# Kernel tuning notes

Measured on AMD Instinct MI355X. Metric: run time of the kernel, lower is better.

Reference implementation:

```python
import jax, jax.numpy as jnp
import numpy as np

B, D, K = 32768, 256, 8192
COMMITMENT_COST = 0.25
DECAY = 0.99
EPS = 1e-05


def setup_inputs() -> dict:
    key = jax.random.key(0)
    k1, k2, k3, k4 = jax.random.split(key, 4)
    z = jax.random.normal(k1, (B, D), dtype=jnp.float32)
    embedding = jax.random.normal(k2, (K, D), dtype=jnp.float32)
    ema_cluster_size = jnp.ones((K,), dtype=jnp.float32)
    ema_embedding_sum = embedding.copy()
    # pre-sampled randomness for dead-code reinitialization (one slot per code)
    reinit_noise = jax.random.normal(k3, (K, D), dtype=jnp.float32) * 0.1
    reinit_idx = jax.random.randint(k4, (K,), 0, B)
    return {
        "z": z,
        "embedding": embedding,
        "ema_cluster_size": ema_cluster_size,
        "ema_embedding_sum": ema_embedding_sum,
        "reinit_noise": reinit_noise,
        "reinit_idx": reinit_idx,
    }


def reference(z, embedding, ema_cluster_size, ema_embedding_sum, reinit_noise, reinit_idx):
    # squared L2 distances: [B, K]
    distances = (
        jnp.sum(z * z, axis=1, keepdims=True)
        + jnp.sum(embedding * embedding, axis=1)
        - 2.0 * jnp.matmul(z, embedding.T)
    )
    indices = jnp.argmin(distances, axis=1)  # [B]
    z_q = embedding[indices]                  # [B, D]

    # EMA codebook update (training-mode math), one-hot scatter via segment_sum
    ones = jnp.ones((z.shape[0],), dtype=z.dtype)
    cluster_size = jax.ops.segment_sum(ones, indices, num_segments=K)       # [K]
    embedding_sum = jax.ops.segment_sum(z, indices, num_segments=K)          # [K, D]
    new_ema_cs = DECAY * ema_cluster_size + (1.0 - DECAY) * cluster_size
    new_ema_es = DECAY * ema_embedding_sum + (1.0 - DECAY) * embedding_sum
    n = jnp.sum(new_ema_cs)
    cs_smoothed = (new_ema_cs + EPS) / (n + K * EPS) * n
    new_embedding = new_ema_es / cs_smoothed[:, None]

    # dead-code reinitialization (masked, fixed-shape)
    usage = new_ema_cs / n
    dead = usage < (1.0 / K / 10.0)           # [K] bool
    reinit = z[reinit_idx] + reinit_noise     # [K, D]
    new_embedding = jnp.where(dead[:, None], reinit, new_embedding)
    new_ema_cs = jnp.where(dead, 1.0, new_ema_cs)
    new_ema_es = jnp.where(dead[:, None], reinit, new_ema_es)

    # losses / metrics
    commitment_loss = COMMITMENT_COST * jnp.mean((jax.lax.stop_gradient(z_q) - z) ** 2)
    z_q_st = z + jax.lax.stop_gradient(z_q - z)  # straight-through
    avg_probs = cluster_size / z.shape[0]
    perplexity = jnp.exp(-jnp.sum(avg_probs * jnp.log(avg_probs + 1e-10)))

    return (z_q_st, commitment_loss, indices, perplexity, new_embedding, new_ema_cs, new_ema_es)
```

## Files before the change

kernel.cpp:

```cpp
#include <hip/hip_runtime.h>
#include <math.h>

#define BN 32768
#define DN 256
#define KN 8192
#define CCAP 20

#define O_LOSS 8388608
#define O_IDX  8388609
#define O_PERP 8421377
#define O_EMB  8421378
#define O_CS   10518530
#define O_ES   10526722

typedef _Float16 half_t;
typedef __attribute__((ext_vector_type(4))) _Float16 half4v;
typedef __attribute__((ext_vector_type(8))) _Float16 half8;
typedef __attribute__((ext_vector_type(16))) float float16v;
typedef unsigned long long u64;
typedef unsigned int u32;

__device__ __forceinline__ float wave_reduce_add(float v) {
#pragma unroll
  for (int off = 32; off > 0; off >>= 1) v += __shfl_down(v, off);
  return v;
}

__device__ __forceinline__ u32 enc_f(float d) {
  u32 fb = __float_as_uint(d);
  return fb ^ ((fb >> 31) ? 0xFFFFFFFFu : 0x80000000u);
}

__global__ __launch_bounds__(256) void k_prep_z(const float* __restrict__ z,
                                                half_t* __restrict__ zh,
                                                float* __restrict__ znh,
                                                float* __restrict__ znl) {
  const int wid = threadIdx.x >> 6, lane = threadIdx.x & 63;
  const int row = blockIdx.x * 4 + wid;
  float4 v = *(const float4*)(z + (size_t)row * DN + lane * 4);
  float xs[4] = {v.x, v.y, v.z, v.w};
  half4v hv;
  float h2 = 0.f, l2 = 0.f;
#pragma unroll
  for (int j = 0; j < 4; ++j) {
    half_t hh = (half_t)xs[j];
    float lf = xs[j] - (float)hh;
    hv[j] = hh;
    h2 += (float)hh * (float)hh;
    l2 += lf * lf;
  }
  const int tile = row >> 7, r = row & 127, kg = lane >> 1, off = (lane & 1) * 4;
  *(half4v*)(zh + (size_t)tile * 32768 + kg * 1024 + r * 8 + off) = hv;
#pragma unroll
  for (int o = 32; o > 0; o >>= 1) {
    h2 += __shfl_down(h2, o);
    l2 += __shfl_down(l2, o);
  }
  if (lane == 0) {
    znh[row] = sqrtf(h2);
    znl[row] = sqrtf(l2);
  }
}

__global__ __launch_bounds__(256) void k_prep_e(const float* __restrict__ e,
                                                half_t* __restrict__ eh,
                                                float* __restrict__ enorm,
                                                float* __restrict__ emaxp) {
  __shared__ float mh[4], ml[4];
  const int wid = threadIdx.x >> 6, lane = threadIdx.x & 63;
  const int row = blockIdx.x * 4 + wid;
  float4 v = *(const float4*)(e + (size_t)row * DN + lane * 4);
  float xs[4] = {v.x, v.y, v.z, v.w};
  half4v hv;
  float h2 = 0.f, l2 = 0.f, x2 = 0.f;
#pragma unroll
  for (int j = 0; j < 4; ++j) {
    half_t hh = (half_t)xs[j];
    float lf = xs[j] - (float)hh;
    hv[j] = hh;
    h2 += (float)hh * (float)hh;
    l2 += lf * lf;
    x2 += xs[j] * xs[j];
  }
  const int tile = row >> 6, r = row & 63, kg = lane >> 1, off = (lane & 1) * 4;
  *(half4v*)(eh + (size_t)tile * 16384 + kg * 512 + r * 8 + off) = hv;
#pragma unroll
  for (int o = 32; o > 0; o >>= 1) {
    h2 += __shfl_down(h2, o);
    l2 += __shfl_down(l2, o);
    x2 += __shfl_down(x2, o);
  }
  if (lane == 0) {
    enorm[row] = x2;
    mh[wid] = sqrtf(h2);
    ml[wid] = sqrtf(l2);
  }
  __syncthreads();
  if (threadIdx.x == 0) {
    emaxp[blockIdx.x * 2] = fmaxf(fmaxf(mh[0], mh[1]), fmaxf(mh[2], mh[3]));
    emaxp[blockIdx.x * 2 + 1] = fmaxf(fmaxf(ml[0], ml[1]), fmaxf(ml[2], ml[3]));
  }
}

__global__ __launch_bounds__(256) void k_norm(const float* __restrict__ emaxp,
                                              float* __restrict__ Wf) {
  __shared__ float sh[256], sl[256];
  const int t = threadIdx.x;
  float vh = 0.f, vl = 0.f;
  for (int i = t; i < 2048; i += 256) {
    vh = fmaxf(vh, emaxp[i * 2]);
    vl = fmaxf(vl, emaxp[i * 2 + 1]);
  }
  sh[t] = vh;
  sl[t] = vl;
  __syncthreads();
  for (int st = 128; st > 0; st >>= 1) {
    if (t < st) {
      sh[t] = fmaxf(sh[t], sh[t + st]);
      sl[t] = fmaxf(sl[t], sl[t + st]);
    }
    __syncthreads();
  }
  if (t == 0) {
    Wf[4] = sh[0];
    Wf[5] = sl[0];
  }
}

__global__ __launch_bounds__(256, 2) void k_pass1(
    const half_t* __restrict__ eh, const half_t* __restrict__ zh,
    const float* __restrict__ z, const float* __restrict__ emb,
    const float* __restrict__ enorm, const float* __restrict__ znh,
    const float* __restrict__ znl, const float* __restrict__ Wf,
    u64* __restrict__ best, u32* __restrict__ oflow) {
  __shared__ __align__(16) half_t EB[2][8192];
  __shared__ float En_s[2048];
  __shared__ u64 clist[128 * CCAP];
  __shared__ u32 pcnt[128];
  __shared__ float rowbest[128];

  const int tid = threadIdx.x;
  const int wid = tid >> 6, lane = tid & 63;
  const int l31 = lane & 31, h = lane >> 5;
  const int zt = blockIdx.x;
  const int sp = blockIdx.y;
  const int lrow = wid * 32 + l31;
  const int grow = zt * 128 + lrow;

  for (int i = tid; i < 2048; i += 256) En_s[i] = enorm[sp * 2048 + i];
  if (tid < 128) pcnt[tid] = 0;

  half8 zr[16];
  {
    const half_t* zb = zh + (size_t)zt * 32768 + (size_t)lrow * 8;
#pragma unroll
    for (int ks = 0; ks < 16; ++ks)
      zr[ks] = *(const half8*)(zb + (size_t)(ks * 2 + h) * 1024);
  }
  const float thr2 =
      4.0f * (znh[grow] * Wf[5] + znl[grow] * (Wf[4] + Wf[5])) + 0.06f;

  const half_t* ebase = eh + ((size_t)sp << 19);
  float bestd = 3.4e38f;

#define STG(s, b)                                                              \
  {                                                                            \
    const half_t* g_ = ebase + (size_t)(s) * 8192 + wid * 2048 + lane * 8;     \
    half_t* d_ = &EB[b][wid * 2048 + lane * 8];                                \
    _Pragma("unroll") for (int i_ = 0; i_ < 4; ++i_)                           \
        __builtin_amdgcn_global_load_lds(                                      \
            (const __attribute__((address_space(1))) void*)(g_ + i_ * 512),    \
            (__attribute__((address_space(3))) void*)(d_ + i_ * 512), 16, 0,   \
            0);                                                                \
  }

  STG(0, 0)
  for (int t = 0; t < 32; ++t) {
    float16v acc0 = {}, acc1 = {};
#pragma unroll
    for (int kh = 0; kh < 2; ++kh) {
      const int s = t * 2 + kh;
      __syncthreads();
      if (s < 63) STG(s + 1, (s + 1) & 1)
      const half_t* B = EB[s & 1];
#pragma unroll
      for (int ks = 0; ks < 8; ++ks) {
        const int ko = (ks * 2 + h) * 512;
        half8 a0 = *(const half8*)(B + ko + l31 * 8);
        half8 a1 = *(const half8*)(B + ko + (32 + l31) * 8);
        acc0 = __builtin_amdgcn_mfma_f32_32x32x16_f16(a0, zr[kh * 8 + ks],
                                                      acc0, 0, 0, 0);
        acc1 = __builtin_amdgcn_mfma_f32_32x32x16_f16(a1, zr[kh * 8 + ks],
                                                      acc1, 0, 0, 0);
      }
    }
    float ds[32];
    float tmin = 3.4e38f;
#pragma unroll
    for (int mi = 0; mi < 2; ++mi) {
      const float16v a = mi ? acc1 : acc0;
#pragma unroll
      for (int r = 0; r < 16; ++r) {
        const int cl = t * 64 + mi * 32 + (r & 3) + 8 * (r >> 2) + 4 * h;
        const float d = En_s[cl] - 2.0f * a[r];
        ds[mi * 16 + r] = d;
        tmin = d < tmin ? d : tmin;
      }
    }
    {
      float o = __shfl_xor(tmin, 32);
      tmin = o < tmin ? o : tmin;
      bestd = tmin < bestd ? tmin : bestd;
    }
    const float lim = bestd + thr2;
#pragma unroll
    for (int mi = 0; mi < 2; ++mi)
#pragma unroll
      for (int r = 0; r < 16; ++r) {
        const float d = ds[mi * 16 + r];
        if (d <= lim) {
          const int cl = t * 64 + mi * 32 + (r & 3) + 8 * (r >> 2) + 4 * h;
          const u32 slot = atomicAdd(&pcnt[lrow], 1u);
          if (slot < CCAP)
            clist[lrow * CCAP + slot] =
                ((u64)enc_f(d) << 32) | (u32)(sp * 2048 + cl);
        }
      }
  }
#undef STG

  if (h == 0) rowbest[lrow] = bestd;
  __syncthreads();

  for (int lr = wid; lr < 128; lr += 4) {
    const int gr = zt * 128 + lr;
    const u32 n = pcnt[lr];
    if (n > CCAP) {
      if (lane == 0) oflow[gr] = 1u;
      continue;
    }
    const float t2 =
        4.0f * (znh[gr] * Wf[5] + znl[gr] * (Wf[4] + Wf[5])) + 0.06f;
    const u32 lim = enc_f(rowbest[lr] + t2);
    u64 bk = ~0ull;
    const float4 zv = *(const float4*)(z + (size_t)gr * DN + lane * 4);
    for (u32 j = 0; j < n; ++j) {
      const u64 e = clist[lr * CCAP + j];
      if ((u32)(e >> 32) > lim) continue;
      const int c = (int)(e & 0x1FFFu);
      float4 ev = *(const float4*)(emb + (size_t)c * DN + lane * 4);
      float dot = wave_reduce_add(zv.x * ev.x + zv.y * ev.y + zv.z * ev.z +
                                  zv.w * ev.w);
      if (lane == 0) {
        const float d = enorm[c] - 2.0f * dot;
        const u64 kk = ((u64)enc_f(d) << 32) | (u32)c;
        bk = kk < bk ? kk : bk;
      }
    }
    if (lane == 0) atomicMin(best + gr, bk);
  }
}

__global__ __launch_bounds__(256) void k_out(const float* __restrict__ z,
                                             const float* __restrict__ emb,
                                             const float* __restrict__ enorm,
                                             const u64* __restrict__ best,
                                             const u32* __restrict__ oflow,
                                             float* __restrict__ out,
                                             float* __restrict__ losspart,
                                             float* __restrict__ cluster,
                                             int* __restrict__ idxp) {
  __shared__ float lp[4];
  int wid = threadIdx.x >> 6, lane = threadIdx.x & 63;
  int row = blockIdx.x * 4 + wid;
  int d = lane << 2;
  float4 zv = *(const float4*)(z + (size_t)row * DN + d);
  int k;
  if (oflow[row] != 0u) {
    u64 bk = ~0ull;
    for (int c = 0; c < KN; ++c) {
      float4 ev = *(const float4*)(emb + (size_t)c * DN + d);
      float dot = wave_reduce_add(zv.x * ev.x + zv.y * ev.y + zv.z * ev.z +
                                  zv.w * ev.w);
      if (lane == 0) {
        const float dd = enorm[c] - 2.0f * dot;
        const u64 kk = ((u64)enc_f(dd) << 32) | (u32)c;
        bk = kk < bk ? kk : bk;
      }
    }
    int k0 = (int)((u32)bk & 0x1FFFu);
    k = __shfl(k0, 0);
  } else {
    k = (int)((u32)best[row] & 0x1FFFu);
  }
  float4 ev = *(const float4*)(emb + (size_t)k * DN + d);
  float4 df = make_float4(ev.x - zv.x, ev.y - zv.y, ev.z - zv.z, ev.w - zv.w);
  float4 st = make_float4(zv.x + df.x, zv.y + df.y, zv.z + df.z, zv.w + df.w);
  *(float4*)(out + (size_t)row * DN + d) = st;
  float sq = df.x * df.x + df.y * df.y + df.z * df.z + df.w * df.w;
  sq = wave_reduce_add(sq);
  if (lane == 0) {
    lp[wid] = sq;
    unsafeAtomicAdd(&cluster[k], 1.0f);
    out[O_IDX + row] = (float)k;
    idxp[row] = k;
  }
  __syncthreads();
  if (threadIdx.x == 0)
    losspart[blockIdx.x] = lp[0] + lp[1] + lp[2] + lp[3];
}

__global__ __launch_bounds__(256) void k_scan(const float* __restrict__ ema_cs,
                                              const float* __restrict__ cluster,
                                              const float* __restrict__ losspart,
                                              float* __restrict__ newcs,
                                              int* __restrict__ rowstart,
                                              int* __restrict__ cursor,
                                              float* __restrict__ Wf) {
  __shared__ int ssum[256];
  __shared__ float sn[256], sp[256], sl[256];
  const int t = threadIdx.x;
  const int base = t * 32;
  int s = 0;
  float nsum = 0.f, plsum = 0.f, lsum = 0.f;
  for (int j = 0; j < 32; ++j) {
    float cs = cluster[base + j];
    s += (int)cs;
    float nc = 0.99f * ema_cs[base + j] + 0.01f * cs;
    newcs[base + j] = nc;
    nsum += nc;
    float p = cs * (1.0f / 32768.0f);
    plsum += p * logf(p + 1e-10f);
    lsum += losspart[base + j];
  }
  ssum[t] = s;
  sn[t] = nsum;
  sp[t] = plsum;
  sl[t] = lsum;
  __syncthreads();
  for (int st = 1; st < 256; st <<= 1) {
    int v = (t >= st) ? ssum[t - st] : 0;
    __syncthreads();
    ssum[t] += v;
    __syncthreads();
  }
  int off = ssum[t] - s;
  for (int j = 0; j < 32; ++j) {
    rowstart[base + j] = off;
    cursor[base + j] = off;
    off += (int)cluster[base + j];
  }
  for (int st = 128; st > 0; st >>= 1) {
    if (t < st) {
      sn[t] += sn[t + st];
      sp[t] += sp[t + st];
      sl[t] += sl[t + st];
    }
    __syncthreads();
  }
  if (t == 0) {
    Wf[0] = sl[0];
    Wf[1] = sn[0];
    Wf[2] = sp[0];
  }
}

__global__ __launch_bounds__(256) void k_scatter(const int* __restrict__ idxp,
                                                 int* __restrict__ cursor,
                                                 int* __restrict__ rowlist) {
  const int row = blockIdx.x * 256 + threadIdx.x;
  const int pos = atomicAdd(cursor + idxp[row], 1);
  rowlist[pos] = row;
}

__global__ __launch_bounds__(256) void k_accum(const float* __restrict__ z,
                                               const float* __restrict__ cluster,
                                               const int* __restrict__ rowstart,
                                               const int* __restrict__ rowlist,
                                               float* __restrict__ embsum) {
  const int wid = threadIdx.x >> 6, lane = threadIdx.x & 63;
  const int code = blockIdx.x * 4 + wid;
  const int cnt = (int)cluster[code];
  const int st = rowstart[code];
  float4 a = make_float4(0.f, 0.f, 0.f, 0.f);
  for (int j = 0; j < cnt; ++j) {
    const int row = rowlist[st + j];
    float4 v = *(const float4*)(z + (size_t)row * DN + lane * 4);
    a.x += v.x;
    a.y += v.y;
    a.z += v.z;
    a.w += v.w;
  }
  *(float4*)(embsum + (size_t)code * DN + lane * 4) = a;
}

__global__ __launch_bounds__(256) void k_final(const float* __restrict__ z,
                                               const float* __restrict__ ema_es,
                                               const float* __restrict__ noise,
                                               const int* __restrict__ ridx,
                                               const float* __restrict__ embsum,
                                               const float* __restrict__ newcs,
                                               const float* __restrict__ W,
                                               float* __restrict__ out) {
  int gid = blockIdx.x * 256 + threadIdx.x;
  int k = gid >> 6;
  int d = (gid & 63) << 2;
  float n = W[1];
  float nc = newcs[k];
  float cs_sm = (nc + 1e-5f) / (n + (float)KN * 1e-5f) * n;
  bool dead = (nc / n) < (1.0f / (KN * 10.0f));
  size_t o = (size_t)k * DN + d;
  float4 es = *(const float4*)(ema_es + o);
  float4 s = *(const float4*)(embsum + o);
  float4 nes = make_float4(0.99f * es.x + 0.01f * s.x, 0.99f * es.y + 0.01f * s.y,
                           0.99f * es.z + 0.01f * s.z, 0.99f * es.w + 0.01f * s.w);
  float4 ne = make_float4(nes.x / cs_sm, nes.y / cs_sm, nes.z / cs_sm,
                          nes.w / cs_sm);
  if (dead) {
    int r = ridx[k];
    float4 rz = *(const float4*)(z + (size_t)r * DN + d);
    float4 rn = *(const float4*)(noise + o);
    nes = make_float4(rz.x + rn.x, rz.y + rn.y, rz.z + rn.z, rz.w + rn.w);
    ne = nes;
  }
  float* oe = out + O_EMB + o;
  *(float2*)(oe) = make_float2(ne.x, ne.y);
  *(float2*)(oe + 2) = make_float2(ne.z, ne.w);
  float* os = out + O_ES + o;
  *(float2*)(os) = make_float2(nes.x, nes.y);
  *(float2*)(os + 2) = make_float2(nes.z, nes.w);
  if ((gid & 63) == 0) out[O_CS + k] = dead ? 1.0f : nc;
  if (gid == 0) {
    out[O_LOSS] = 0.25f * W[0] * (1.0f / 8388608.0f);
    out[O_PERP] = expf(-W[2]);
  }
}

extern "C" void kernel_launch(void* const* d_in, const int* in_sizes, int n_in,
                              void* d_out, int out_size, void* d_ws,
                              size_t ws_size, hipStream_t stream) {
  const float* z = (const float*)d_in[0];
  const float* emb = (const float*)d_in[1];
  const float* ema_cs = (const float*)d_in[2];
  const float* ema_es = (const float*)d_in[3];
  const float* noise = (const float*)d_in[4];
  const int* ridx = (const int*)d_in[5];
  float* out = (float*)d_out;

  float* Wf = (float*)d_ws;
  float* cluster = Wf + 16;
  u32* oflow = (u32*)(cluster + KN);
  float* newcs = (float*)(oflow + BN);
  float* enorm = newcs + KN;
  float* znh = enorm + KN;
  float* znl = znh + BN;
  int* rowstart = (int*)(znl + BN);
  int* cursor = rowstart + KN;
  int* rowlist = cursor + KN;
  int* idxp = rowlist + BN;
  float* losspart = (float*)(idxp + BN);
  float* emaxp = losspart + KN;
  u64* best = (u64*)(emaxp + 4096);
  float* embsum = (float*)(best + BN);

  half_t* zh = (half_t*)out;
  half_t* eh = (half_t*)(out + (size_t)BN * DN / 2);

  hipMemsetAsync(Wf, 0, (size_t)(16 + KN + BN) * sizeof(float), stream);
  hipMemsetAsync(best, 0xFF, (size_t)BN * sizeof(u64), stream);

  k_prep_z<<<BN / 4, 256, 0, stream>>>(z, zh, znh, znl);
  k_prep_e<<<KN / 4, 256, 0, stream>>>(emb, eh, enorm, emaxp);
  k_norm<<<1, 256, 0, stream>>>(emaxp, Wf);
  k_pass1<<<dim3(BN / 128, 4), 256, 0, stream>>>(eh, zh, z, emb, enorm, znh,
                                                 znl, Wf, best, oflow);
  k_out<<<BN / 4, 256, 0, stream>>>(z, emb, enorm, best, oflow, out, losspart,
                                    cluster, idxp);
  k_scan<<<1, 256, 0, stream>>>(ema_cs, cluster, losspart, newcs, rowstart,
                                cursor, Wf);
  k_scatter<<<BN / 256, 256, 0, stream>>>(idxp, cursor, rowlist);
  k_accum<<<KN / 4, 256, 0, stream>>>(z, cluster, rowstart, rowlist, embsum);
  k_final<<<(KN * 64) / 256, 256, 0, stream>>>(z, ema_es, noise, ridx, embsum,
                                               newcs, Wf, out);
}
```

Baseline: 637.1 us.

## Restructure distance GEMM to register-resident z tiles with per-wave codebook slices

The pass-1 distance kernel now processes 64 z rows per block, with two 32-row z fragments held in registers. Each wave streams its own 512-code slice of the half-precision codebook straight from global memory instead of sharing double-buffered LDS stages behind block-wide barriers. Per-row best distances are shared across waves through LDS atomicMin so candidate pruning stays tight, and the candidate cap is raised. The z and codebook prep kernels are merged into one launch using a shared 64-row tile layout. This removes LDS staging and barriers, but each block now rereads the codebook from global memory or L2 with no LDS reuse, and there are more blocks.

```diff
diff --git a/kernel.cpp b/kernel.cpp
--- a/kernel.cpp
+++ b/kernel.cpp
@@ -4,7 +4,7 @@
 #define BN 32768
 #define DN 256
 #define KN 8192
-#define CCAP 20
+#define CCAP 24
 
 #define O_LOSS 8388608
 #define O_IDX  8388609
@@ -30,46 +30,24 @@
   u32 fb = __float_as_uint(d);
   return fb ^ ((fb >> 31) ? 0xFFFFFFFFu : 0x80000000u);
 }
-
-__global__ __launch_bounds__(256) void k_prep_z(const float* __restrict__ z,
-                                                half_t* __restrict__ zh,
-                                                float* __restrict__ znh,
-                                                float* __restrict__ znl) {
-  const int wid = threadIdx.x >> 6, lane = threadIdx.x & 63;
-  const int row = blockIdx.x * 4 + wid;
-  float4 v = *(const float4*)(z + (size_t)row * DN + lane * 4);
-  float xs[4] = {v.x, v.y, v.z, v.w};
-  half4v hv;
-  float h2 = 0.f, l2 = 0.f;
-#pragma unroll
-  for (int j = 0; j < 4; ++j) {
-    half_t hh = (half_t)xs[j];
-    float lf = xs[j] - (float)hh;
-    hv[j] = hh;
-    h2 += (float)hh * (float)hh;
-    l2 += lf * lf;
-  }
-  const int tile = row >> 7, r = row & 127, kg = lane >> 1, off = (lane & 1) * 4;
-  *(half4v*)(zh + (size_t)tile * 32768 + kg * 1024 + r * 8 + off) = hv;
-#pragma unroll
-  for (int o = 32; o > 0; o >>= 1) {
-    h2 += __shfl_down(h2, o);
-    l2 += __shfl_down(l2, o);
-  }
-  if (lane == 0) {
-    znh[row] = sqrtf(h2);
-    znl[row] = sqrtf(l2);
-  }
-}
-
-__global__ __launch_bounds__(256) void k_prep_e(const float* __restrict__ e,
-                                                half_t* __restrict__ eh,
-                                                float* __restrict__ enorm,
-                                                float* __restrict__ emaxp) {
+__device__ __forceinline__ float dec_key(u32 u) {
+  return __uint_as_float((u & 0x80000000u) ? (u ^ 0x80000000u) : ~u);
+}
+
+__global__ __launch_bounds__(256) void k_prep(const float* __restrict__ z,
+                                              const float* __restrict__ e,
+                                              half_t* __restrict__ zh,
+                                              half_t* __restrict__ eh,
+                                              float* __restrict__ znh,
+                                              float* __restrict__ znl,
+                                              float* __restrict__ enorm,
+                                              float* __restrict__ emaxp) {
   __shared__ float mh[4], ml[4];
   const int wid = threadIdx.x >> 6, lane = threadIdx.x & 63;
-  const int row = blockIdx.x * 4 + wid;
-  float4 v = *(const float4*)(e + (size_t)row * DN + lane * 4);
+  const bool is_z = blockIdx.x < 8192;
+  const int row = (is_z ? blockIdx.x : blockIdx.x - 8192) * 4 + wid;
+  const float* src = is_z ? z : e;
+  float4 v = *(const float4*)(src + (size_t)row * DN + lane * 4);
   float xs[4] = {v.x, v.y, v.z, v.w};
   half4v hv;
   float h2 = 0.f, l2 = 0.f, x2 = 0.f;
@@ -83,22 +61,31 @@
     x2 += xs[j] * xs[j];
   }
   const int tile = row >> 6, r = row & 63, kg = lane >> 1, off = (lane & 1) * 4;
-  *(half4v*)(eh + (size_t)tile * 16384 + kg * 512 + r * 8 + off) = hv;
+  half_t* dst = is_z ? zh : eh;
+  *(half4v*)(dst + (size_t)tile * 16384 + kg * 512 + r * 8 + off) = hv;
 #pragma unroll
   for (int o = 32; o > 0; o >>= 1) {
     h2 += __shfl_down(h2, o);
     l2 += __shfl_down(l2, o);
     x2 += __shfl_down(x2, o);
   }
-  if (lane == 0) {
-    enorm[row] = x2;
-    mh[wid] = sqrtf(h2);
-    ml[wid] = sqrtf(l2);
-  }
-  __syncthreads();
-  if (threadIdx.x == 0) {
-    emaxp[blockIdx.x * 2] = fmaxf(fmaxf(mh[0], mh[1]), fmaxf(mh[2], mh[3]));
-    emaxp[blockIdx.x * 2 + 1] = fmaxf(fmaxf(ml[0], ml[1]), fmaxf(ml[2], ml[3]));
+  if (is_z) {
+    if (lane == 0) {
+      znh[row] = sqrtf(h2);
+      znl[row] = sqrtf(l2);
+    }
+  } else {
+    if (lane == 0) {
+      enorm[row] = x2;
+      mh[wid] = sqrtf(h2);
+      ml[wid] = sqrtf(l2);
+    }
+    __syncthreads();
+    if (threadIdx.x == 0) {
+      const int b = blockIdx.x - 8192;
+      emaxp[b * 2] = fmaxf(fmaxf(mh[0], mh[1]), fmaxf(mh[2], mh[3]));
+      emaxp[b * 2 + 1] = fmaxf(fmaxf(ml[0], ml[1]), fmaxf(ml[2], ml[3]));
+    }
   }
 }
 
@@ -133,120 +120,113 @@
     const float* __restrict__ enorm, const float* __restrict__ znh,
     const float* __restrict__ znl, const float* __restrict__ Wf,
     u64* __restrict__ best, u32* __restrict__ oflow) {
-  __shared__ __align__(16) half_t EB[2][8192];
   __shared__ float En_s[2048];
-  __shared__ u64 clist[128 * CCAP];
-  __shared__ u32 pcnt[128];
-  __shared__ float rowbest[128];
+  __shared__ u64 clist[64 * CCAP];
+  __shared__ u32 pcnt[64];
+  __shared__ u32 rbest[64];
 
   const int tid = threadIdx.x;
   const int wid = tid >> 6, lane = tid & 63;
   const int l31 = lane & 31, h = lane >> 5;
   const int zt = blockIdx.x;
   const int sp = blockIdx.y;
-  const int lrow = wid * 32 + l31;
-  const int grow = zt * 128 + lrow;
 
   for (int i = tid; i < 2048; i += 256) En_s[i] = enorm[sp * 2048 + i];
-  if (tid < 128) pcnt[tid] = 0;
-
-  half8 zr[16];
+  if (tid < 64) {
+    pcnt[tid] = 0;
+    rbest[tid] = 0xFFFFFFFFu;
+  }
+
+  half8 zr0[16], zr1[16];
   {
-    const half_t* zb = zh + (size_t)zt * 32768 + (size_t)lrow * 8;
-#pragma unroll
-    for (int ks = 0; ks < 16; ++ks)
-      zr[ks] = *(const half8*)(zb + (size_t)(ks * 2 + h) * 1024);
-  }
-  const float thr2 =
-      4.0f * (znh[grow] * Wf[5] + znl[grow] * (Wf[4] + Wf[5])) + 0.06f;
-
-  const half_t* ebase = eh + ((size_t)sp << 19);
-  float bestd = 3.4e38f;
-
-#define STG(s, b)                                                              \
-  {                                                                            \
-    const half_t* g_ = ebase + (size_t)(s) * 8192 + wid * 2048 + lane * 8;     \
-    half_t* d_ = &EB[b][wid * 2048 + lane * 8];                                \
-    _Pragma("unroll") for (int i_ = 0; i_ < 4; ++i_)                           \
-        __builtin_amdgcn_global_load_lds(                                      \
-            (const __attribute__((address_space(1))) void*)(g_ + i_ * 512),    \
-            (__attribute__((address_space(3))) void*)(d_ + i_ * 512), 16, 0,   \
-            0);                                                                \
-  }
-
-  STG(0, 0)
-  for (int t = 0; t < 32; ++t) {
-    float16v acc0 = {}, acc1 = {};
-#pragma unroll
-    for (int kh = 0; kh < 2; ++kh) {
-      const int s = t * 2 + kh;
-      __syncthreads();
-      if (s < 63) STG(s + 1, (s + 1) & 1)
-      const half_t* B = EB[s & 1];
-#pragma unroll
-      for (int ks = 0; ks < 8; ++ks) {
-        const int ko = (ks * 2 + h) * 512;
-        half8 a0 = *(const half8*)(B + ko + l31 * 8);
-        half8 a1 = *(const half8*)(B + ko + (32 + l31) * 8);
-        acc0 = __builtin_amdgcn_mfma_f32_32x32x16_f16(a0, zr[kh * 8 + ks],
-                                                      acc0, 0, 0, 0);
-        acc1 = __builtin_amdgcn_mfma_f32_32x32x16_f16(a1, zr[kh * 8 + ks],
-                                                      acc1, 0, 0, 0);
+    const half_t* zb = zh + (size_t)zt * 16384;
+#pragma unroll
+    for (int kt = 0; kt < 16; ++kt) {
+      zr0[kt] = *(const half8*)(zb + (2 * kt + h) * 512 + l31 * 8);
+      zr1[kt] = *(const half8*)(zb + (2 * kt + h) * 512 + (32 + l31) * 8);
+    }
+  }
+  const int gr0 = zt * 64 + l31, gr1 = gr0 + 32;
+  const float maxEh = Wf[4], maxEl = Wf[5];
+  const float thr0 = 4.0f * (znh[gr0] * maxEl + znl[gr0] * (maxEh + maxEl)) + 0.06f;
+  const float thr1 = 4.0f * (znh[gr1] * maxEl + znl[gr1] * (maxEh + maxEl)) + 0.06f;
+  __syncthreads();
+
+  const int cq = wid * 512;
+  float bd0 = 3.4e38f, bd1 = 3.4e38f;
+
+  for (int ct = 0; ct < 16; ++ct) {
+    const int cbase = cq + ct * 32;
+    const int gc0 = sp * 2048 + cbase;
+    const half_t* ab =
+        eh + (size_t)(gc0 >> 6) * 16384 + (size_t)(gc0 & 63) * 8;
+    float16v a0 = {}, a1 = {};
+#pragma unroll
+    for (int kt = 0; kt < 16; ++kt) {
+      half8 af = *(const half8*)(ab + (2 * kt + h) * 512 + l31 * 8);
+      a0 = __builtin_amdgcn_mfma_f32_32x32x16_f16(af, zr0[kt], a0, 0, 0, 0);
+      a1 = __builtin_amdgcn_mfma_f32_32x32x16_f16(af, zr1[kt], a1, 0, 0, 0);
+    }
+    float t0 = 3.4e38f, t1 = 3.4e38f;
+#pragma unroll
+    for (int r = 0; r < 16; ++r) {
+      const float en = En_s[cbase + (r & 3) + 8 * (r >> 2) + 4 * h];
+      const float d0 = en - 2.0f * a0[r];
+      const float d1 = en - 2.0f * a1[r];
+      t0 = d0 < t0 ? d0 : t0;
+      t1 = d1 < t1 ? d1 : t1;
+    }
+    {
+      float o0 = __shfl_xor(t0, 32), o1 = __shfl_xor(t1, 32);
+      t0 = o0 < t0 ? o0 : t0;
+      t1 = o1 < t1 ? o1 : t1;
+      bd0 = t0 < bd0 ? t0 : bd0;
+      bd1 = t1 < bd1 ? t1 : bd1;
+      if (h == 0) {
+        atomicMin(&rbest[l31], enc_f(bd0));
+        atomicMin(&rbest[32 + l31], enc_f(bd1));
       }
     }
-    float ds[32];
-    float tmin = 3.4e38f;
-#pragma unroll
-    for (int mi = 0; mi < 2; ++mi) {
-      const float16v a = mi ? acc1 : acc0;
-#pragma unroll
-      for (int r = 0; r < 16; ++r) {
-        const int cl = t * 64 + mi * 32 + (r & 3) + 8 * (r >> 2) + 4 * h;
-        const float d = En_s[cl] - 2.0f * a[r];
-        ds[mi * 16 + r] = d;
-        tmin = d < tmin ? d : tmin;
+    const float lim0 = fminf(bd0, dec_key(rbest[l31])) + thr0;
+    const float lim1 = fminf(bd1, dec_key(rbest[32 + l31])) + thr1;
+#pragma unroll
+    for (int r = 0; r < 16; ++r) {
+      const int cl = cbase + (r & 3) + 8 * (r >> 2) + 4 * h;
+      const float en = En_s[cl];
+      const float d0 = en - 2.0f * a0[r];
+      const float d1 = en - 2.0f * a1[r];
+      if (d0 <= lim0) {
+        const u32 slot = atomicAdd(&pcnt[l31], 1u);
+        if (slot < CCAP)
+          clist[l31 * CCAP + slot] =
+              ((u64)enc_f(d0) << 32) | (u32)(sp * 2048 + cl);
       }
-    }
-    {
-      float o = __shfl_xor(tmin, 32);
-      tmin = o < tmin ? o : tmin;
-      bestd = tmin < bestd ? tmin : bestd;
-    }
-    const float lim = bestd + thr2;
-#pragma unroll
-    for (int mi = 0; mi < 2; ++mi)
-#pragma unroll
-      for (int r = 0; r < 16; ++r) {
-        const float d = ds[mi * 16 + r];
-        if (d <= lim) {
-          const int cl = t * 64 + mi * 32 + (r & 3) + 8 * (r >> 2) + 4 * h;
-          const u32 slot = atomicAdd(&pcnt[lrow], 1u);
-          if (slot < CCAP)
-            clist[lrow * CCAP + slot] =
-                ((u64)enc_f(d) << 32) | (u32)(sp * 2048 + cl);
-        }
+      if (d1 <= lim1) {
+        const u32 slot = atomicAdd(&pcnt[32 + l31], 1u);
+        if (slot < CCAP)
+          clist[(32 + l31) * CCAP + slot] =
+              ((u64)enc_f(d1) << 32) | (u32)(sp * 2048 + cl);
       }
-  }
-#undef STG
-
-  if (h == 0) rowbest[lrow] = bestd;
+    }
+  }
   __syncthreads();
 
-  for (int lr = wid; lr < 128; lr += 4) {
-    const int gr = zt * 128 + lr;
+  for (int i = 0; i < 16; ++i) {
+    const int lr = wid * 16 + i;
+    const int gr = zt * 64 + lr;
     const u32 n = pcnt[lr];
     if (n > CCAP) {
       if (lane == 0) oflow[gr] = 1u;
       continue;
     }
     const float t2 =
-        4.0f * (znh[gr] * Wf[5] + znl[gr] * (Wf[4] + Wf[5])) + 0.06f;
-    const u32 lim = enc_f(rowbest[lr] + t2);
+        4.0f * (znh[gr] * maxEl + znl[gr] * (maxEh + maxEl)) + 0.06f;
+    const u32 limu = enc_f(dec_key(rbest[lr]) + t2);
     u64 bk = ~0ull;
     const float4 zv = *(const float4*)(z + (size_t)gr * DN + lane * 4);
     for (u32 j = 0; j < n; ++j) {
       const u64 e = clist[lr * CCAP + j];
-      if ((u32)(e >> 32) > lim) continue;
+      if ((u32)(e >> 32) > limu) continue;
       const int c = (int)(e & 0x1FFFu);
       float4 ev = *(const float4*)(emb + (size_t)c * DN + lane * 4);
       float dot = wave_reduce_add(zv.x * ev.x + zv.y * ev.y + zv.z * ev.z +
@@ -469,11 +449,11 @@
   hipMemsetAsync(Wf, 0, (size_t)(16 + KN + BN) * sizeof(float), stream);
   hipMemsetAsync(best, 0xFF, (size_t)BN * sizeof(u64), stream);
 
-  k_prep_z<<<BN / 4, 256, 0, stream>>>(z, zh, znh, znl);
-  k_prep_e<<<KN / 4, 256, 0, stream>>>(emb, eh, enorm, emaxp);
+  k_prep<<<BN / 4 + KN / 4, 256, 0, stream>>>(z, emb, zh, eh, znh, znl, enorm,
+                                              emaxp);
   k_norm<<<1, 256, 0, stream>>>(emaxp, Wf);
-  k_pass1<<<dim3(BN / 128, 4), 256, 0, stream>>>(eh, zh, z, emb, enorm, znh,
-                                                 znl, Wf, best, oflow);
+  k_pass1<<<dim3(BN / 64, 4), 256, 0, stream>>>(eh, zh, z, emb, enorm, znh,
+                                                znl, Wf, best, oflow);
   k_out<<<BN / 4, 256, 0, stream>>>(z, emb, enorm, best, oflow, out, losspart,
                                     cluster, idxp);
   k_scan<<<1, 256, 0, stream>>>(ema_cs, cluster, losspart, newcs, rowstart,
```

Result: slower. 706.5 us (+10.9%).
